# Kernel optimization log

Measured on AMD Instinct MI355X. Metric: run time of the kernel, lower is better.

The kernel has to match this reference:

```python
import jax, jax.numpy as jnp
import numpy as np

B, T_DEC, T_SRC, D = 32, 1024, 2048, 1024


def setup_inputs() -> dict:
    key = jax.random.key(0)
    k1, k2, k3 = jax.random.split(key, 3)
    decoder_outputs = jax.random.normal(k1, (B, T_DEC, D), dtype=jnp.float32)
    encoder_outputs = jax.random.normal(k2, (B, T_SRC, D), dtype=jnp.float32)
    # realistic padding mask: each batch element has a valid length in [T_SRC//2, T_SRC]
    lengths = jax.random.randint(k3, (B, 1, 1), T_SRC // 2, T_SRC + 1)
    src_mask = jnp.arange(T_SRC)[None, None, :] < lengths  # [B,1,T_SRC] bool
    return {"decoder_outputs": decoder_outputs, "encoder_outputs": encoder_outputs, "src_mask": src_mask}


def reference(decoder_outputs, encoder_outputs, src_mask):
    # scores: [B, T_dec, T_src]
    scores = jnp.einsum('btd,bsd->bts', decoder_outputs, encoder_outputs)
    scores = jnp.where(src_mask, scores, -jnp.inf)  # src_mask [B,1,T_src] broadcasts over T_dec
    attn_weights = jax.nn.softmax(scores, axis=-1)
    context = jnp.einsum('bts,bsd->btd', attn_weights, encoder_outputs)
    return context, attn_weights
```

## Files before the change

### kernel.cpp

```cpp
#include <hip/hip_runtime.h>
#include <stdint.h>

#define NB 32
#define TDEC 1024
#define TSRC 2048
#define DDIM 1024

typedef short bf16x8 __attribute__((ext_vector_type(8)));
typedef float f32x4 __attribute__((ext_vector_type(4)));


__device__ __forceinline__ unsigned short f2bf(float f) {
  union { float f; uint32_t u; } c; c.f = f;
  return (unsigned short)((c.u + 0x7FFFu + ((c.u >> 16) & 1u)) >> 16);
}

__device__ __forceinline__ void splitt(float f, unsigned short& h, unsigned short& l) {
  union { float f; uint32_t u; } c; c.f = f;
  uint32_t hb = c.u & 0xFFFF0000u;
  h = (unsigned short)(hb >> 16);
  union { uint32_t u; float f; } hf; hf.u = hb;
  union { float f; uint32_t u; } d; d.f = f - hf.f;
  l = (unsigned short)(d.u >> 16);
}

__device__ __forceinline__ int sw4(int r, int c4) {
  return (r << 6) + ((((c4 >> 3) ^ (r & 7)) << 3) | (c4 & 7));
}
__device__ __forceinline__ int sw8(int r, int c8) {
  return (r << 6) + (((c8 >> 3) ^ (r & 7)) << 3);
}

__device__ __forceinline__ void gload16(const void* g, void* l) {
  __builtin_amdgcn_global_load_lds(
      reinterpret_cast<const __attribute__((address_space(1))) uint32_t*>(
          reinterpret_cast<uintptr_t>(g)),
      reinterpret_cast<__attribute__((address_space(3))) uint32_t*>(
          reinterpret_cast<uintptr_t>(l)),
      16, 0, 0);
}

__global__ void lens_kernel(const unsigned char* __restrict__ mask,
                            int* __restrict__ lens) {
  int b = blockIdx.x;
  int tid = threadIdx.x;
  unsigned char b1 = mask[1], b3 = mask[3];
  int cnt = 0;
  if (b1 != 0) {
    const unsigned char* row = mask + (size_t)b * TSRC;
    for (int s = tid; s < TSRC; s += 256) cnt += (row[s] != 0) ? 1 : 0;
  } else if (b3 != 0) {
    const float* row = (const float*)mask + (size_t)b * TSRC;
    for (int s = tid; s < TSRC; s += 256) cnt += (row[s] != 0.0f) ? 1 : 0;
  } else {
    const int* row = (const int*)mask + (size_t)b * TSRC;
    for (int s = tid; s < TSRC; s += 256) cnt += (row[s] != 0) ? 1 : 0;
  }
#pragma unroll
  for (int o = 32; o > 0; o >>= 1) cnt += __shfl_down(cnt, o, 64);
  __shared__ int red[4];
  if ((tid & 63) == 0) red[tid >> 6] = cnt;
  __syncthreads();
  if (tid == 0) lens[b] = red[0] + red[1] + red[2] + red[3];
}

__global__ void split_kernel(const float* __restrict__ src,
                             unsigned short* __restrict__ hi,
                             unsigned short* __restrict__ lo, int n4) {
  int i = blockIdx.x * 256 + threadIdx.x;
  if (i >= n4) return;
  float4 v = *(const float4*)(src + (size_t)i * 4);
  ushort4 h, l;
  splitt(v.x, h.x, l.x); splitt(v.y, h.y, l.y);
  splitt(v.z, h.z, l.z); splitt(v.w, h.w, l.w);
  *(ushort4*)(hi + (size_t)i * 4) = h;
  *(ushort4*)(lo + (size_t)i * 4) = l;
}

__global__ void encprep_kernel(const float* __restrict__ enc,
                               unsigned short* __restrict__ ehi,
                               unsigned short* __restrict__ elo,
                               unsigned short* __restrict__ encT) {
  __shared__ float tile[64][65];
  int b = blockIdx.z;
  int s0 = blockIdx.x << 6;
  int d0 = blockIdx.y << 6;
  int tid = threadIdx.x;
  int rl = tid >> 4;
  int c4 = (tid & 15) << 2;
  const float* src = enc + ((size_t)b * TSRC + s0) * DDIM + d0;
  unsigned short* hdst = ehi + ((size_t)b * TSRC + s0) * DDIM + d0;
  unsigned short* ldst = elo + ((size_t)b * TSRC + s0) * DDIM + d0;
#pragma unroll
  for (int p = 0; p < 4; ++p) {
    int s = rl + (p << 4);
    float4 v = *(const float4*)(src + (size_t)s * DDIM + c4);
    tile[s][c4 + 0] = v.x; tile[s][c4 + 1] = v.y;
    tile[s][c4 + 2] = v.z; tile[s][c4 + 3] = v.w;
    ushort4 h, l;
    splitt(v.x, h.x, l.x); splitt(v.y, h.y, l.y);
    splitt(v.z, h.z, l.z); splitt(v.w, h.w, l.w);
    *(ushort4*)(hdst + (size_t)s * DDIM + c4) = h;
    *(ushort4*)(ldst + (size_t)s * DDIM + c4) = l;
  }
  __syncthreads();
  unsigned short* dst = encT + ((size_t)b * DDIM + d0) * TSRC + s0;
#pragma unroll
  for (int p = 0; p < 4; ++p) {
    int d = rl + (p << 4);
    ushort4 o;
    o.x = f2bf(tile[c4 + 0][d]);
    o.y = f2bf(tile[c4 + 1][d]);
    o.z = f2bf(tile[c4 + 2][d]);
    o.w = f2bf(tile[c4 + 3][d]);
    *(ushort4*)(dst + (size_t)d * TSRC + c4) = o;
  }
}

__global__ __launch_bounds__(256, 2) void scores_pre(
    const unsigned short* __restrict__ dhi, const unsigned short* __restrict__ dlo,
    const unsigned short* __restrict__ ehi, const unsigned short* __restrict__ elo,
    float* __restrict__ attn, const int* __restrict__ lens) {
  int b = blockIdx.z;
  int s0 = blockIdx.x << 7;
  int t0 = blockIdx.y << 7;
  if (s0 >= lens[b]) return;
  __shared__ __align__(16) unsigned short As[2][8192], Bs[2][8192];
  const unsigned short* Ag0 = dhi + ((size_t)b * TDEC + t0) * DDIM;
  const unsigned short* Ag1 = dlo + ((size_t)b * TDEC + t0) * DDIM;
  const unsigned short* Bg0 = ehi + ((size_t)b * TSRC + s0) * DDIM;
  const unsigned short* Bg1 = elo + ((size_t)b * TSRC + s0) * DDIM;
  int tid = threadIdx.x;
  int lane = tid & 63, wid = tid >> 6;
  int wm = (wid >> 1) << 6, wn = (wid & 1) << 6;
  int fr = lane & 15, fq = lane >> 4;

  int gg[4]; size_t go[4];
#pragma unroll
  for (int p = 0; p < 4; ++p) {
    int g = (p << 8) + tid;
    int r = g >> 3;
    int sg = (g & 7) ^ (r & 7);
    gg[p] = g << 3;
    go[p] = (size_t)r * DDIM + (sg << 3);
  }

  f32x4 acc[16];
#pragma unroll
  for (int i = 0; i < 16; ++i) { acc[i][0] = 0.f; acc[i][1] = 0.f; acc[i][2] = 0.f; acc[i][3] = 0.f; }

  auto stage = [&](int buf, int kc) {
    const unsigned short* Ab = (kc >= 16 && kc < 32) ? Ag1 : Ag0;
    const unsigned short* Bb = (kc >= 32) ? Bg1 : Bg0;
    int k0 = (kc & 15) << 6;
    unsigned short* Ad = &As[buf][0];
    unsigned short* Bd = &Bs[buf][0];
#pragma unroll
    for (int p = 0; p < 4; ++p) {
      gload16(Ab + go[p] + k0, Ad + gg[p]);
      gload16(Bb + go[p] + k0, Bd + gg[p]);
    }
  };

  auto compute = [&](int buf) {
    const unsigned short* At = &As[buf][0];
    const unsigned short* Bt = &Bs[buf][0];
#pragma unroll
    for (int ks = 0; ks < 2; ++ks) {
      bf16x8 a[4], bb[4];
#pragma unroll
      for (int i = 0; i < 4; ++i) {
        int ra = wm + (i << 4) + fr;
        a[i] = *(const bf16x8*)&At[(ra << 6) + ((((ks << 2) | fq) ^ (ra & 7)) << 3)];
        int rb = wn + (i << 4) + fr;
        bb[i] = *(const bf16x8*)&Bt[(rb << 6) + ((((ks << 2) | fq) ^ (rb & 7)) << 3)];
      }
#pragma unroll
      for (int mt = 0; mt < 4; ++mt)
#pragma unroll
        for (int nt = 0; nt < 4; ++nt)
          acc[(mt << 2) + nt] = __builtin_amdgcn_mfma_f32_16x16x32_bf16(
              a[mt], bb[nt], acc[(mt << 2) + nt], 0, 0, 0);
    }
  };

  stage(0, 0);
  int cur = 0;
  for (int kc = 0; kc < 47; ++kc) {
    stage(cur ^ 1, kc + 1);
    asm volatile("s_waitcnt vmcnt(8)" ::: "memory");
    __builtin_amdgcn_s_barrier();
    __builtin_amdgcn_sched_barrier(0);
    compute(cur);
    __builtin_amdgcn_sched_barrier(0);
    __builtin_amdgcn_s_barrier();
    cur ^= 1;
  }
  asm volatile("s_waitcnt vmcnt(0)" ::: "memory");
  __builtin_amdgcn_s_barrier();
  __builtin_amdgcn_sched_barrier(0);
  compute(cur);

  float* C = attn + ((size_t)b * TDEC + t0) * TSRC + s0;
#pragma unroll
  for (int mt = 0; mt < 4; ++mt) {
    int r0 = wm + (mt << 4) + (fq << 2);
#pragma unroll
    for (int nt = 0; nt < 4; ++nt) {
      int c0 = wn + (nt << 4) + fr;
      f32x4 v = acc[(mt << 2) + nt];
#pragma unroll
      for (int j = 0; j < 4; ++j)
        C[(size_t)(r0 + j) * TSRC + c0] = v[j];
    }
  }
}

__global__ __launch_bounds__(256, 2) void scores_fly(
    const float* __restrict__ dec, const float* __restrict__ enc,
    float* __restrict__ attn, const int* __restrict__ lens) {
  int b = blockIdx.z;
  int s0 = blockIdx.x << 7;
  int t0 = blockIdx.y << 7;
  if (s0 >= lens[b]) return;
  __shared__ unsigned short Ah[8192], Al[8192], Bh[8192], Bl[8192];
  const float* Ag = dec + ((size_t)b * TDEC + t0) * DDIM;
  const float* Bg = enc + ((size_t)b * TSRC + s0) * DDIM;
  int tid = threadIdx.x;
  int lane = tid & 63, wid = tid >> 6;
  int wm = (wid >> 1) << 6, wn = (wid & 1) << 6;
  int fr = lane & 15, fq = lane >> 4;

  f32x4 acc[16];
#pragma unroll
  for (int i = 0; i < 16; ++i) { acc[i][0] = 0.f; acc[i][1] = 0.f; acc[i][2] = 0.f; acc[i][3] = 0.f; }

  for (int kc = 0; kc < 16; ++kc) {
    int k0 = kc << 6;
    __syncthreads();
#pragma unroll
    for (int p = 0; p < 8; ++p) {
      int r = (p << 4) + (tid >> 4);
      int c4 = (tid & 15) << 2;
      size_t go = (size_t)r * DDIM + k0 + c4;
      float4 va = *(const float4*)(Ag + go);
      float4 vb = *(const float4*)(Bg + go);
      ushort4 h, l;
      splitt(va.x, h.x, l.x); splitt(va.y, h.y, l.y);
      splitt(va.z, h.z, l.z); splitt(va.w, h.w, l.w);
      int sw = sw4(r, c4);
      *(ushort4*)&Ah[sw] = h; *(ushort4*)&Al[sw] = l;
      splitt(vb.x, h.x, l.x); splitt(vb.y, h.y, l.y);
      splitt(vb.z, h.z, l.z); splitt(vb.w, h.w, l.w);
      *(ushort4*)&Bh[sw] = h; *(ushort4*)&Bl[sw] = l;
    }
    __syncthreads();
#pragma unroll
    for (int ks = 0; ks < 2; ++ks) {
      bf16x8 ah[4], al[4], bh[4], bl[4];
#pragma unroll
      for (int i = 0; i < 4; ++i) {
        int ra = wm + (i << 4) + fr;
        int oa = (ra << 6) + ((((ks << 2) | fq) ^ (ra & 7)) << 3);
        ah[i] = *(const bf16x8*)&Ah[oa];
        al[i] = *(const bf16x8*)&Al[oa];
        int rb = wn + (i << 4) + fr;
        int ob = (rb << 6) + ((((ks << 2) | fq) ^ (rb & 7)) << 3);
        bh[i] = *(const bf16x8*)&Bh[ob];
        bl[i] = *(const bf16x8*)&Bl[ob];
      }
#pragma unroll
      for (int mt = 0; mt < 4; ++mt)
#pragma unroll
        for (int nt = 0; nt < 4; ++nt) {
          f32x4 c = acc[(mt << 2) + nt];
          c = __builtin_amdgcn_mfma_f32_16x16x32_bf16(ah[mt], bh[nt], c, 0, 0, 0);
          c = __builtin_amdgcn_mfma_f32_16x16x32_bf16(al[mt], bh[nt], c, 0, 0, 0);
          c = __builtin_amdgcn_mfma_f32_16x16x32_bf16(ah[mt], bl[nt], c, 0, 0, 0);
          acc[(mt << 2) + nt] = c;
        }
    }
  }
  float* C = attn + ((size_t)b * TDEC + t0) * TSRC + s0;
#pragma unroll
  for (int mt = 0; mt < 4; ++mt) {
    int r0 = wm + (mt << 4) + (fq << 2);
#pragma unroll
    for (int nt = 0; nt < 4; ++nt) {
      int c0 = wn + (nt << 4) + fr;
      f32x4 v = acc[(mt << 2) + nt];
#pragma unroll
      for (int j = 0; j < 4; ++j)
        C[(size_t)(r0 + j) * TSRC + c0] = v[j];
    }
  }
}

__global__ __launch_bounds__(256) void softmax_kernel(float* __restrict__ attn,
                                                      const int* __restrict__ lens,
                                                      unsigned short* __restrict__ attn_bf) {
  int b = blockIdx.y;
  int t = blockIdx.x;
  int len = lens[b];
  float* row = attn + ((size_t)b * TDEC + t) * TSRC;
  int tid = threadIdx.x;
  int p0 = tid << 2;
  int p1 = 1024 + (tid << 2);
  float4 v0 = *(const float4*)(row + p0);
  float4 v1 = *(const float4*)(row + p1);
  float x[8] = {v0.x, v0.y, v0.z, v0.w, v1.x, v1.y, v1.z, v1.w};
  float m = -3.4e38f;
#pragma unroll
  for (int j = 0; j < 8; ++j) {
    int pos = (j < 4) ? (p0 + j) : (p1 + j - 4);
    if (pos < len) m = fmaxf(m, x[j]);
  }
#pragma unroll
  for (int o = 32; o > 0; o >>= 1) m = fmaxf(m, __shfl_down(m, o, 64));
  __shared__ float redm[4], reds[4];
  if ((tid & 63) == 0) redm[tid >> 6] = m;
  __syncthreads();
  m = fmaxf(fmaxf(redm[0], redm[1]), fmaxf(redm[2], redm[3]));
  float e[8];
  float s = 0.f;
#pragma unroll
  for (int j = 0; j < 8; ++j) {
    int pos = (j < 4) ? (p0 + j) : (p1 + j - 4);
    float ev = (pos < len) ? __expf(x[j] - m) : 0.f;
    e[j] = ev;
    s += ev;
  }
#pragma unroll
  for (int o = 32; o > 0; o >>= 1) s += __shfl_down(s, o, 64);
  if ((tid & 63) == 0) reds[tid >> 6] = s;
  __syncthreads();
  s = reds[0] + reds[1] + reds[2] + reds[3];
  float inv = 1.0f / s;
  float4 o0, o1;
  o0.x = e[0] * inv; o0.y = e[1] * inv; o0.z = e[2] * inv; o0.w = e[3] * inv;
  o1.x = e[4] * inv; o1.y = e[5] * inv; o1.z = e[6] * inv; o1.w = e[7] * inv;
  *(float4*)(row + p0) = o0;
  *(float4*)(row + p1) = o1;
  if (attn_bf) {
    unsigned short* rb = attn_bf + ((size_t)b * TDEC + t) * TSRC;
    ushort4 h0, h1;
    h0.x = f2bf(o0.x); h0.y = f2bf(o0.y); h0.z = f2bf(o0.z); h0.w = f2bf(o0.w);
    h1.x = f2bf(o1.x); h1.y = f2bf(o1.y); h1.z = f2bf(o1.z); h1.w = f2bf(o1.w);
    *(ushort4*)(rb + p0) = h0;
    *(ushort4*)(rb + p1) = h1;
  }
}

__global__ __launch_bounds__(256, 2) void context_pre(
    const unsigned short* __restrict__ attn_bf, const unsigned short* __restrict__ encT,
    float* __restrict__ ctx, const int* __restrict__ lens) {
  int b = blockIdx.z;
  int d0 = blockIdx.x << 7;
  int t0 = blockIdx.y << 7;
  int nk = (lens[b] + 63) >> 6;
  __shared__ __align__(16) unsigned short As[2][8192], Bs[2][8192];
  const unsigned short* Ag = attn_bf + ((size_t)b * TDEC + t0) * TSRC;
  const unsigned short* Bg = encT + ((size_t)b * DDIM + d0) * TSRC;
  int tid = threadIdx.x;
  int lane = tid & 63, wid = tid >> 6;
  int wm = (wid >> 1) << 6, wn = (wid & 1) << 6;
  int fr = lane & 15, fq = lane >> 4;

  int gg[4]; size_t go[4];
#pragma unroll
  for (int p = 0; p < 4; ++p) {
    int g = (p << 8) + tid;
    int r = g >> 3;
    int sg = (g & 7) ^ (r & 7);
    gg[p] = g << 3;
    go[p] = (size_t)r * TSRC + (sg << 3);
  }

  f32x4 acc[16];
#pragma unroll
  for (int i = 0; i < 16; ++i) { acc[i][0] = 0.f; acc[i][1] = 0.f; acc[i][2] = 0.f; acc[i][3] = 0.f; }

  auto stage = [&](int buf, int kc) {
    int k0 = kc << 6;
    unsigned short* Ad = &As[buf][0];
    unsigned short* Bd = &Bs[buf][0];
#pragma unroll
    for (int p = 0; p < 4; ++p) {
      gload16(Ag + go[p] + k0, Ad + gg[p]);
      gload16(Bg + go[p] + k0, Bd + gg[p]);
    }
  };

  auto compute = [&](int buf) {
    const unsigned short* At = &As[buf][0];
    const unsigned short* Bt = &Bs[buf][0];
#pragma unroll
    for (int ks = 0; ks < 2; ++ks) {
      bf16x8 a[4], bb[4];
#pragma unroll
      for (int i = 0; i < 4; ++i) {
        int ra = wm + (i << 4) + fr;
        a[i] = *(const bf16x8*)&At[(ra << 6) + ((((ks << 2) | fq) ^ (ra & 7)) << 3)];
        int rb = wn + (i << 4) + fr;
        bb[i] = *(const bf16x8*)&Bt[(rb << 6) + ((((ks << 2) | fq) ^ (rb & 7)) << 3)];
      }
#pragma unroll
      for (int mt = 0; mt < 4; ++mt)
#pragma unroll
        for (int nt = 0; nt < 4; ++nt)
          acc[(mt << 2) + nt] = __builtin_amdgcn_mfma_f32_16x16x32_bf16(
              a[mt], bb[nt], acc[(mt << 2) + nt], 0, 0, 0);
    }
  };

  stage(0, 0);
  int cur = 0;
  for (int kc = 0; kc < nk - 1; ++kc) {
    stage(cur ^ 1, kc + 1);
    asm volatile("s_waitcnt vmcnt(8)" ::: "memory");
    __builtin_amdgcn_s_barrier();
    __builtin_amdgcn_sched_barrier(0);
    compute(cur);
    __builtin_amdgcn_sched_barrier(0);
    __builtin_amdgcn_s_barrier();
    cur ^= 1;
  }
  asm volatile("s_waitcnt vmcnt(0)" ::: "memory");
  __builtin_amdgcn_s_barrier();
  __builtin_amdgcn_sched_barrier(0);
  compute(cur);

  float* C = ctx + ((size_t)b * TDEC + t0) * DDIM + d0;
#pragma unroll
  for (int mt = 0; mt < 4; ++mt) {
    int r0 = wm + (mt << 4) + (fq << 2);
#pragma unroll
    for (int nt = 0; nt < 4; ++nt) {
      int c0 = wn + (nt << 4) + fr;
      f32x4 v = acc[(mt << 2) + nt];
#pragma unroll
      for (int j = 0; j < 4; ++j)
        C[(size_t)(r0 + j) * DDIM + c0] = v[j];
    }
  }
}

__global__ __launch_bounds__(256, 2) void context_fly(
    const float* __restrict__ attn, const float* __restrict__ enc,
    float* __restrict__ ctx, const int* __restrict__ lens) {
  int b = blockIdx.z;
  int d0 = blockIdx.x << 7;
  int t0 = blockIdx.y << 7;
  int nk = (lens[b] + 63) >> 6;
  __shared__ unsigned short At[8192], Bt[8192];
  const float* Ag = attn + ((size_t)b * TDEC + t0) * TSRC;
  const float* Bg = enc + (size_t)b * TSRC * DDIM + d0;
  int tid = threadIdx.x;
  int lane = tid & 63, wid = tid >> 6;
  int wm = (wid >> 1) << 6, wn = (wid & 1) << 6;
  int fr = lane & 15, fq = lane >> 4;

  f32x4 acc[16];
#pragma unroll
  for (int i = 0; i < 16; ++i) { acc[i][0] = 0.f; acc[i][1] = 0.f; acc[i][2] = 0.f; acc[i][3] = 0.f; }

  for (int kc = 0; kc < nk; ++kc) {
    int k0 = kc << 6;
    __syncthreads();
#pragma unroll
    for (int p = 0; p < 8; ++p) {
      int r = (p << 4) + (tid >> 4);
      int c4 = (tid & 15) << 2;
      float4 v = *(const float4*)(Ag + (size_t)r * TSRC + k0 + c4);
      ushort4 h;
      h.x = f2bf(v.x); h.y = f2bf(v.y); h.z = f2bf(v.z); h.w = f2bf(v.w);
      *(ushort4*)&At[sw4(r, c4)] = h;
    }
#pragma unroll
    for (int p = 0; p < 8; ++p) {
      int idx = (p << 8) + tid;
      int sl = idx >> 5;
      int d4 = (idx & 31) << 2;
      float4 v = *(const float4*)(Bg + (size_t)(k0 + sl) * DDIM + d4);
      float tmp[4] = {v.x, v.y, v.z, v.w};
#pragma unroll
      for (int j = 0; j < 4; ++j) {
        int n = d4 + j;
        Bt[(n << 6) + ((((sl >> 3) ^ (n & 7)) << 3) | (sl & 7))] = f2bf(tmp[j]);
      }
    }
    __syncthreads();
#pragma unroll
    for (int ks = 0; ks < 2; ++ks) {
      bf16x8 a[4], bb[4];
#pragma unroll
      for (int i = 0; i < 4; ++i) {
        int ra = wm + (i << 4) + fr;
        a[i] = *(const bf16x8*)&At[(ra << 6) + ((((ks << 2) | fq) ^ (ra & 7)) << 3)];
        int rb = wn + (i << 4) + fr;
        bb[i] = *(const bf16x8*)&Bt[(rb << 6) + ((((ks << 2) | fq) ^ (rb & 7)) << 3)];
      }
#pragma unroll
      for (int mt = 0; mt < 4; ++mt)
#pragma unroll
        for (int nt = 0; nt < 4; ++nt)
          acc[(mt << 2) + nt] = __builtin_amdgcn_mfma_f32_16x16x32_bf16(
              a[mt], bb[nt], acc[(mt << 2) + nt], 0, 0, 0);
    }
  }
  float* C = ctx + ((size_t)b * TDEC + t0) * DDIM + d0;
#pragma unroll
  for (int mt = 0; mt < 4; ++mt) {
    int r0 = wm + (mt << 4) + (fq << 2);
#pragma unroll
    for (int nt = 0; nt < 4; ++nt) {
      int c0 = wn + (nt << 4) + fr;
      f32x4 v = acc[(mt << 2) + nt];
#pragma unroll
      for (int j = 0; j < 4; ++j)
        C[(size_t)(r0 + j) * DDIM + c0] = v[j];
    }
  }
}

extern "C" void kernel_launch(void* const* d_in, const int* in_sizes, int n_in,
                              void* d_out, int out_size, void* d_ws, size_t ws_size,
                              hipStream_t stream) {
  (void)in_sizes; (void)n_in; (void)out_size;
  const float* dec = (const float*)d_in[0];
  const float* enc = (const float*)d_in[1];
  const unsigned char* mask = (const unsigned char*)d_in[2];
  float* ctx = (float*)d_out;
  float* attn = ctx + (size_t)NB * TDEC * DDIM;

  size_t nDec = (size_t)NB * TDEC * DDIM;
  size_t nEnc = (size_t)NB * TSRC * DDIM;
  char* wsb = (char*)d_ws;
  int* lens = (int*)wsb;
  unsigned short* dec_hi = (unsigned short*)(wsb + 256);
  unsigned short* dec_lo = dec_hi + nDec;
  unsigned short* enc_hi = dec_lo + nDec;
  unsigned short* enc_lo = enc_hi + nEnc;
  unsigned short* encT = enc_lo + nEnc;
  unsigned short* attn_bf = dec_hi;
  size_t need = 256 + (2 * nDec + 3 * nEnc) * sizeof(unsigned short);
  int pre = (ws_size >= need) ? 1 : 0;

  lens_kernel<<<NB, 256, 0, stream>>>(mask, lens);
  if (pre) {
    split_kernel<<<(int)(nDec / 4 / 256), 256, 0, stream>>>(dec, dec_hi, dec_lo, (int)(nDec / 4));
    encprep_kernel<<<dim3(TSRC / 64, DDIM / 64, NB), 256, 0, stream>>>(enc, enc_hi, enc_lo, encT);
    scores_pre<<<dim3(TSRC / 128, TDEC / 128, NB), 256, 0, stream>>>(
        dec_hi, dec_lo, enc_hi, enc_lo, attn, lens);
  } else {
    scores_fly<<<dim3(TSRC / 128, TDEC / 128, NB), 256, 0, stream>>>(dec, enc, attn, lens);
  }
  softmax_kernel<<<dim3(TDEC, NB), 256, 0, stream>>>(attn, lens, pre ? attn_bf : (unsigned short*)nullptr);
  if (pre) {
    context_pre<<<dim3(DDIM / 128, TDEC / 128, NB), 256, 0, stream>>>(attn_bf, encT, ctx, lens);
  } else {
    context_fly<<<dim3(DDIM / 128, TDEC / 128, NB), 256, 0, stream>>>(attn, enc, ctx, lens);
  }
}
```

Measured before the change: 1.299 ms.

## Enlarge scores GEMM tile to 256x256 with 4-stage pipeline and block swizzle

Rewrites the split-bf16 scores GEMM to use 256x256 output tiles with 512 threads (8 waves, each computing 128x64), K-step of 32, and a 4-slot shared-memory ring with loads issued three steps ahead and a single barrier per step. It also adds a 1D grid with a block-index swizzle for locality and setprio around the MFMA bursts. The aim is more data reuse per global load and better overlap of loads with MFMA; the cost is higher register and LDS use (one block per CU) and coarser early-exit granularity for masked columns.

```diff
diff --git a/kernel.cpp b/kernel.cpp
--- a/kernel.cpp
+++ b/kernel.cpp
@@ -117,98 +117,108 @@
   }
 }
 
-__global__ __launch_bounds__(256, 2) void scores_pre(
+#define SC_NSUB 96
+__global__ __launch_bounds__(512, 1) void scores_pre(
     const unsigned short* __restrict__ dhi, const unsigned short* __restrict__ dlo,
     const unsigned short* __restrict__ ehi, const unsigned short* __restrict__ elo,
     float* __restrict__ attn, const int* __restrict__ lens) {
-  int b = blockIdx.z;
-  int s0 = blockIdx.x << 7;
-  int t0 = blockIdx.y << 7;
+  int lid = blockIdx.x;
+  int swz = ((lid & 7) << 7) + (lid >> 3);
+  int sx = swz & 7, sy = (swz >> 3) & 3, b = swz >> 5;
+  int s0 = sx << 8, t0 = sy << 8;
   if (s0 >= lens[b]) return;
-  __shared__ __align__(16) unsigned short As[2][8192], Bs[2][8192];
-  const unsigned short* Ag0 = dhi + ((size_t)b * TDEC + t0) * DDIM;
-  const unsigned short* Ag1 = dlo + ((size_t)b * TDEC + t0) * DDIM;
-  const unsigned short* Bg0 = ehi + ((size_t)b * TSRC + s0) * DDIM;
-  const unsigned short* Bg1 = elo + ((size_t)b * TSRC + s0) * DDIM;
+  __shared__ __align__(16) unsigned short As[4][8192], Bs[4][8192];
+  const unsigned short* Ah_ = dhi + ((size_t)b * TDEC + t0) * DDIM;
+  const unsigned short* Al_ = dlo + ((size_t)b * TDEC + t0) * DDIM;
+  const unsigned short* Bh_ = ehi + ((size_t)b * TSRC + s0) * DDIM;
+  const unsigned short* Bl_ = elo + ((size_t)b * TSRC + s0) * DDIM;
   int tid = threadIdx.x;
   int lane = tid & 63, wid = tid >> 6;
-  int wm = (wid >> 1) << 6, wn = (wid & 1) << 6;
+  int wm = (wid >> 2) << 7;
+  int wn = (wid & 3) << 6;
   int fr = lane & 15, fq = lane >> 4;
 
-  int gg[4]; size_t go[4];
-#pragma unroll
-  for (int p = 0; p < 4; ++p) {
-    int g = (p << 8) + tid;
-    int r = g >> 3;
-    int sg = (g & 7) ^ (r & 7);
-    gg[p] = g << 3;
-    go[p] = (size_t)r * DDIM + (sg << 3);
-  }
-
-  f32x4 acc[16];
-#pragma unroll
-  for (int i = 0; i < 16; ++i) { acc[i][0] = 0.f; acc[i][1] = 0.f; acc[i][2] = 0.f; acc[i][3] = 0.f; }
-
-  auto stage = [&](int buf, int kc) {
-    const unsigned short* Ab = (kc >= 16 && kc < 32) ? Ag1 : Ag0;
-    const unsigned short* Bb = (kc >= 32) ? Bg1 : Bg0;
-    int k0 = (kc & 15) << 6;
-    unsigned short* Ad = &As[buf][0];
-    unsigned short* Bd = &Bs[buf][0];
-#pragma unroll
-    for (int p = 0; p < 4; ++p) {
-      gload16(Ab + go[p] + k0, Ad + gg[p]);
-      gload16(Bb + go[p] + k0, Bd + gg[p]);
+  int gg[2]; size_t go[2];
+#pragma unroll
+  for (int q = 0; q < 2; ++q) {
+    int g = (q << 9) + tid;
+    int r = g >> 2;
+    int sg = (g & 3) ^ ((r >> 1) & 3);
+    gg[q] = g << 3;
+    go[q] = (size_t)r * DDIM + (sg << 3);
+  }
+
+  f32x4 acc[8][4];
+#pragma unroll
+  for (int i = 0; i < 8; ++i)
+#pragma unroll
+    for (int n = 0; n < 4; ++n) { acc[i][n][0] = 0.f; acc[i][n][1] = 0.f; acc[i][n][2] = 0.f; acc[i][n][3] = 0.f; }
+
+  auto stage = [&](int s) {
+    const unsigned short* Asrc = (s >= 32 && s < 64) ? Al_ : Ah_;
+    const unsigned short* Bsrc = (s >= 64) ? Bl_ : Bh_;
+    int k0 = (s & 31) << 5;
+    int slot = s & 3;
+#pragma unroll
+    for (int q = 0; q < 2; ++q) {
+      gload16(Asrc + go[q] + k0, &As[slot][gg[q]]);
+      gload16(Bsrc + go[q] + k0, &Bs[slot][gg[q]]);
     }
   };
 
-  auto compute = [&](int buf) {
-    const unsigned short* At = &As[buf][0];
-    const unsigned short* Bt = &Bs[buf][0];
-#pragma unroll
-    for (int ks = 0; ks < 2; ++ks) {
-      bf16x8 a[4], bb[4];
-#pragma unroll
-      for (int i = 0; i < 4; ++i) {
-        int ra = wm + (i << 4) + fr;
-        a[i] = *(const bf16x8*)&At[(ra << 6) + ((((ks << 2) | fq) ^ (ra & 7)) << 3)];
-        int rb = wn + (i << 4) + fr;
-        bb[i] = *(const bf16x8*)&Bt[(rb << 6) + ((((ks << 2) | fq) ^ (rb & 7)) << 3)];
-      }
-#pragma unroll
-      for (int mt = 0; mt < 4; ++mt)
-#pragma unroll
-        for (int nt = 0; nt < 4; ++nt)
-          acc[(mt << 2) + nt] = __builtin_amdgcn_mfma_f32_16x16x32_bf16(
-              a[mt], bb[nt], acc[(mt << 2) + nt], 0, 0, 0);
-    }
-  };
-
-  stage(0, 0);
-  int cur = 0;
-  for (int kc = 0; kc < 47; ++kc) {
-    stage(cur ^ 1, kc + 1);
-    asm volatile("s_waitcnt vmcnt(8)" ::: "memory");
-    __builtin_amdgcn_s_barrier();
-    __builtin_amdgcn_sched_barrier(0);
-    compute(cur);
-    __builtin_amdgcn_sched_barrier(0);
-    __builtin_amdgcn_s_barrier();
-    cur ^= 1;
-  }
-  asm volatile("s_waitcnt vmcnt(0)" ::: "memory");
+  stage(0); stage(1); stage(2);
+  asm volatile("s_waitcnt vmcnt(8)" ::: "memory");
   __builtin_amdgcn_s_barrier();
-  __builtin_amdgcn_sched_barrier(0);
-  compute(cur);
+
+  for (int s = 0; s < SC_NSUB; ++s) {
+    int slot = s & 3;
+    const unsigned short* At = &As[slot][0];
+    const unsigned short* Bt = &Bs[slot][0];
+    bf16x8 bfr[4], afr[8];
+#pragma unroll
+    for (int n = 0; n < 4; ++n) {
+      int rb = wn + (n << 4) + fr;
+      bfr[n] = *(const bf16x8*)&Bt[(rb << 5) + ((fq ^ ((rb >> 1) & 3)) << 3)];
+    }
+#pragma unroll
+    for (int i = 0; i < 4; ++i) {
+      int ra = wm + (i << 4) + fr;
+      afr[i] = *(const bf16x8*)&At[(ra << 5) + ((fq ^ ((ra >> 1) & 3)) << 3)];
+    }
+    if (s + 3 < SC_NSUB) stage(s + 3);
+    __builtin_amdgcn_s_setprio(1);
+#pragma unroll
+    for (int i = 0; i < 4; ++i)
+#pragma unroll
+      for (int n = 0; n < 4; ++n)
+        acc[i][n] = __builtin_amdgcn_mfma_f32_16x16x32_bf16(afr[i], bfr[n], acc[i][n], 0, 0, 0);
+    __builtin_amdgcn_s_setprio(0);
+#pragma unroll
+    for (int i = 4; i < 8; ++i) {
+      int ra = wm + (i << 4) + fr;
+      afr[i] = *(const bf16x8*)&At[(ra << 5) + ((fq ^ ((ra >> 1) & 3)) << 3)];
+    }
+    __builtin_amdgcn_s_setprio(1);
+#pragma unroll
+    for (int i = 4; i < 8; ++i)
+#pragma unroll
+      for (int n = 0; n < 4; ++n)
+        acc[i][n] = __builtin_amdgcn_mfma_f32_16x16x32_bf16(afr[i], bfr[n], acc[i][n], 0, 0, 0);
+    __builtin_amdgcn_s_setprio(0);
+    if (s < SC_NSUB - 3)       asm volatile("s_waitcnt vmcnt(8)" ::: "memory");
+    else if (s == SC_NSUB - 3) asm volatile("s_waitcnt vmcnt(4)" ::: "memory");
+    else if (s == SC_NSUB - 2) asm volatile("s_waitcnt vmcnt(0)" ::: "memory");
+    if (s < SC_NSUB - 1) __builtin_amdgcn_s_barrier();
+  }
 
   float* C = attn + ((size_t)b * TDEC + t0) * TSRC + s0;
 #pragma unroll
-  for (int mt = 0; mt < 4; ++mt) {
-    int r0 = wm + (mt << 4) + (fq << 2);
-#pragma unroll
-    for (int nt = 0; nt < 4; ++nt) {
-      int c0 = wn + (nt << 4) + fr;
-      f32x4 v = acc[(mt << 2) + nt];
+  for (int i = 0; i < 8; ++i) {
+    int r0 = wm + (i << 4) + (fq << 2);
+#pragma unroll
+    for (int n = 0; n < 4; ++n) {
+      int c0 = wn + (n << 4) + fr;
+      f32x4 v = acc[i][n];
 #pragma unroll
       for (int j = 0; j < 4; ++j)
         C[(size_t)(r0 + j) * TSRC + c0] = v[j];
@@ -550,7 +560,7 @@
   if (pre) {
     split_kernel<<<(int)(nDec / 4 / 256), 256, 0, stream>>>(dec, dec_hi, dec_lo, (int)(nDec / 4));
     encprep_kernel<<<dim3(TSRC / 64, DDIM / 64, NB), 256, 0, stream>>>(enc, enc_hi, enc_lo, encT);
-    scores_pre<<<dim3(TSRC / 128, TDEC / 128, NB), 256, 0, stream>>>(
+    scores_pre<<<dim3((TSRC / 256) * (TDEC / 256) * NB), 512, 0, stream>>>(
         dec_hi, dec_lo, enc_hi, enc_lo, attn, lens);
   } else {
     scores_fly<<<dim3(TSRC / 128, TDEC / 128, NB), 256, 0, stream>>>(dec, enc, attn, lens);
```

After: 1.280 ms. No clear change (-1.4%).
